# Performance work log

Hardware: AMD Instinct MI355X
Metric: run time of the kernel (lower is better)

## Reference

```python
import jax, jax.numpy as jnp
import numpy as np

EPS = 1e-5

def _causal_conv(x, w):
    # x: [B, Cin, S], w: [Cout, Cin, K]; left-pad by K-1 for causality
    k = w.shape[-1]
    x = jnp.pad(x, ((0, 0), (0, 0), (k - 1, 0)))
    return jax.lax.conv_general_dilated(x, w, (1,), 'VALID',
                                        dimension_numbers=('NCH', 'OIH', 'NCH'))

def _activate_norm(x):
    # relu -> mean-center over last axis -> scaled L2 normalize over last axis
    x = jax.nn.relu(x)
    x = x - x.mean(-1, keepdims=True)
    n = x.shape[-1]
    denom = (jnp.sqrt(jnp.sum(x * x, axis=-1, keepdims=True)) + EPS) * (n ** -0.5)
    return x / denom

def _feed_forward(x, w0, w1, w2):
    x = _causal_conv(x, w0)
    x = _activate_norm(x)
    x = _causal_conv(x, w1)
    x = _activate_norm(x)
    return _causal_conv(x, w2)

def setup_inputs() -> dict:
    key = jax.random.key(0)
    B, F, S = 4, 1024, 2048
    I, K = 2048, 5
    ks = jax.random.split(key, 12)
    def w(k, shape):
        fan_in = shape[1] * shape[2]
        return jax.random.normal(k, shape, jnp.float32) * (fan_in ** -0.5)
    inp = jax.random.normal(ks[0], (B, F, S), jnp.float32)
    pos_embd = jax.random.normal(ks[1], (1, F, S), jnp.float32) * 0.02
    divisor = jax.random.uniform(ks[2], (1, F, S), jnp.float32) + 0.5  # bounded away from 0
    return {
        'inp': inp, 'pos_embd': pos_embd, 'divisor': divisor,
        'dw0': w(ks[3], (I, F, 1)), 'dw1': w(ks[4], (I, I, K)), 'dw2': w(ks[5], (F, I, 1)),
        'sw0': w(ks[6], (I, F, 1)), 'sw1': w(ks[7], (I, I, K)), 'sw2': w(ks[8], (F, I, 1)),
        'hw0': w(ks[9], (I, F, 1)), 'hw1': w(ks[10], (I, I, K)), 'hw2': w(ks[11], (F, I, 1)),
    }

def reference(inp, pos_embd, divisor, dw0, dw1, dw2, sw0, sw1, sw2, hw0, hw1, hw2):
    out = inp + pos_embd
    depth = _feed_forward(out, dw0, dw1, dw2)
    scale = _feed_forward(out, sw0, sw1, sw2)
    shift = _feed_forward(out, hw0, hw1, hw2)
    # linear attention: cumsum over dim 1 (as in source), divide, scale/shift, norm, residual
    return inp + _activate_norm(jnp.cumsum(depth, axis=1) / divisor * scale + shift)
```

## Files before the change

### kernel.cpp

```cpp
#include <hip/hip_runtime.h>
#include <math.h>

#define BSZ 4
#define FCH 1024
#define SEQ 2048
#define ICH 2048
#define KW  5
#define EPSV 1e-5f
#define RPAD 2244
#define NCHUNK 16

typedef __attribute__((ext_vector_type(8))) short bf16x8;
typedef __attribute__((ext_vector_type(4))) float f32x4;
typedef __attribute__((ext_vector_type(4))) unsigned short us4;

__device__ __forceinline__ unsigned short f2bf(float f) {
  union { float f; unsigned u; } v; v.f = f;
  unsigned r = v.u + 0x7fff + ((v.u >> 16) & 1);
  return (unsigned short)(r >> 16);
}

__device__ __forceinline__ void gload_lds16(const void* g, void* l) {
  __builtin_amdgcn_global_load_lds(
      (const __attribute__((address_space(1))) void*)g,
      (__attribute__((address_space(3))) void*)l, 16, 0, 0);
}

__global__ __launch_bounds__(256) void addpos_T_kernel(
    const float* __restrict__ inp, const float* __restrict__ pos,
    unsigned short* __restrict__ X)
{
  __shared__ float t[64][65];
  const int s0 = blockIdx.x * 64, f0 = blockIdx.y * 64, b = blockIdx.z;
  const int a = threadIdx.x & 63, g = threadIdx.x >> 6;
  const float* ib = inp + (size_t)b * FCH * SEQ;
#pragma unroll
  for (int i = 0; i < 16; ++i) {
    const size_t o = (size_t)(f0 + g + i * 4) * SEQ + s0 + a;
    t[a][g + i * 4] = ib[o] + pos[o];
  }
  __syncthreads();
#pragma unroll
  for (int i = 0; i < 16; ++i)
    X[(size_t)b * RPAD * FCH + (size_t)(4 + s0 + g + i * 4) * FCH + f0 + a] =
        f2bf(t[g + i * 4][a]);
}

__global__ __launch_bounds__(256) void zero_xpad_kernel(unsigned short* __restrict__ X)
{
  const int i = blockIdx.x * 256 + threadIdx.x;
  const int b = i / (4 * FCH);
  const int r = i % (4 * FCH);
  X[(size_t)b * RPAD * FCH + r] = 0;
}

__global__ __launch_bounds__(256) void transpose_div_kernel(
    const float* __restrict__ D, float* __restrict__ O)
{
  __shared__ float t[64][65];
  const int s0 = blockIdx.x * 64, f0 = blockIdx.y * 64;
  const int a = threadIdx.x & 63, g = threadIdx.x >> 6;
#pragma unroll
  for (int i = 0; i < 16; ++i)
    t[a][g + i * 4] = D[(size_t)(f0 + g + i * 4) * SEQ + s0 + a];
  __syncthreads();
#pragma unroll
  for (int i = 0; i < 16; ++i)
    O[(size_t)(s0 + g + i * 4) * FCH + f0 + a] = t[g + i * 4][a];
}

__global__ __launch_bounds__(256) void cast_bf_kernel(
    const float* __restrict__ I, unsigned short* __restrict__ O)
{
  const size_t i = ((size_t)blockIdx.x * 256 + threadIdx.x) * 4;
  const float4 v = *(const float4*)(I + i);
  us4 o; o.x = f2bf(v.x); o.y = f2bf(v.y); o.z = f2bf(v.z); o.w = f2bf(v.w);
  *(us4*)(O + i) = o;
}

__global__ __launch_bounds__(256) void cast_w1_kernel(
    const float* __restrict__ W, unsigned short* __restrict__ O)
{
  const int c = blockIdx.x * 256 + threadIdx.x;
  const int m = blockIdx.y;
  const float* s = W + ((size_t)m * ICH + c) * KW;
#pragma unroll
  for (int k = 0; k < KW; ++k)
    O[((size_t)k * ICH + m) * ICH + c] = f2bf(s[k]);
}

template <int BN, int NTAPS>
__global__ __launch_bounds__(512, 2) void gemm256_kernel(
    const unsigned short* __restrict__ A, const unsigned short* __restrict__ W,
    float* __restrict__ C, int M, int K)
{
  extern __shared__ __align__(16) char lds[];
  constexpr int ABYTES = 32768;
  constexpr int BBYTES = BN * 128;
  constexpr int BUF = ABYTES + BBYTES;
  constexpr int WN  = BN / 4;
  constexpr int JF  = BN / 64;
  constexpr int JF2 = BN / 128;

  const int tid = threadIdx.x;
  const int ln  = tid & 63;
  const int wv  = tid >> 6;
  const int wr  = wv >> 2;
  const int wc  = wv & 3;
  const int l15 = ln & 15;
  const int lhi = ln >> 4;

  const int s0 = blockIdx.x * 256;
  const int m0 = blockIdx.y * BN;
  const int b  = blockIdx.z;

  const char* Ab = (const char*)(A + (size_t)b * RPAD * K);
  const char* Wb = (const char*)W;
  const size_t MK = (size_t)M * K;
  const int KT = K >> 6;

  const int scs  = (((tid & 7) ^ ((tid >> 3) & 7)) << 4);
  const int rxor = (l15 & 7) << 4;
  const int cbx0 = (lhi * 16) ^ rxor;
  const int cbx1 = (lhi * 16 + 64) ^ rxor;

  f32x4 acc[8][JF] = {};

  auto STAGE = [&](int t, int k0, int pb) {
    const int roff = (NTAPS == 1) ? 4 : t;
    char* dst = lds + pb * BUF;
#pragma unroll
    for (int q = 0; q < 4; ++q) {
      const int row = (q * 512 + tid) >> 3;
      gload_lds16(Ab + (size_t)(s0 + row + roff) * ((size_t)K * 2) +
                      (size_t)(k0 * 2 + scs),
                  dst + q * 8192 + tid * 16);
    }
#pragma unroll
    for (int q = 0; q < BN / 64; ++q) {
      const int row = (q * 512 + tid) >> 3;
      gload_lds16(Wb + ((size_t)t * MK + (size_t)(m0 + row) * K + k0) * 2 + scs,
                  dst + ABYTES + q * 8192 + tid * 16);
    }
  };

  auto COMPUTE = [&](int pb) {
    const char* bb = lds + pb * BUF;
#pragma unroll
    for (int ih = 0; ih < 2; ++ih) {
      bf16x8 af[4][2];
#pragma unroll
      for (int i = 0; i < 4; ++i) {
        const int r = (wr * 128 + ih * 64 + i * 16 + l15) * 128;
        af[i][0] = *(const bf16x8*)(bb + r + cbx0);
        af[i][1] = *(const bf16x8*)(bb + r + cbx1);
      }
#pragma unroll
      for (int jh = 0; jh < 2; ++jh) {
        bf16x8 bfr[JF2][2];
#pragma unroll
        for (int j = 0; j < JF2; ++j) {
          const int r = ABYTES + (wc * WN + jh * (WN / 2) + j * 16 + l15) * 128;
          bfr[j][0] = *(const bf16x8*)(bb + r + cbx0);
          bfr[j][1] = *(const bf16x8*)(bb + r + cbx1);
        }
        __builtin_amdgcn_s_setprio(1);
#pragma unroll
        for (int i = 0; i < 4; ++i)
#pragma unroll
          for (int j = 0; j < JF2; ++j) {
            acc[ih * 4 + i][jh * JF2 + j] = __builtin_amdgcn_mfma_f32_16x16x32_bf16(
                af[i][0], bfr[j][0], acc[ih * 4 + i][jh * JF2 + j], 0, 0, 0);
            acc[ih * 4 + i][jh * JF2 + j] = __builtin_amdgcn_mfma_f32_16x16x32_bf16(
                af[i][1], bfr[j][1], acc[ih * 4 + i][jh * JF2 + j], 0, 0, 0);
          }
        __builtin_amdgcn_s_setprio(0);
      }
    }
  };

  STAGE(0, 0, 0);
  asm volatile("s_waitcnt vmcnt(0)" ::: "memory");
  __syncthreads();
  int p = 0;
  for (int t = 0; t < NTAPS; ++t) {
    for (int kt = 0; kt < KT; ++kt) {
      int ntp = t, nk = kt + 1;
      if (nk == KT) { nk = 0; ++ntp; }
      if (ntp < NTAPS) STAGE(ntp, nk * 64, p ^ 1);
      COMPUTE(p);
      asm volatile("s_waitcnt vmcnt(0)" ::: "memory");
      __syncthreads();
      p ^= 1;
    }
  }

  float* Cb = C + (size_t)b * SEQ * M;
#pragma unroll
  for (int i = 0; i < 8; ++i) {
    const int sb = s0 + wr * 128 + i * 16 + lhi * 4;
#pragma unroll
    for (int j = 0; j < JF; ++j) {
      const int m = m0 + wc * WN + j * 16 + l15;
#pragma unroll
      for (int r = 0; r < 4; ++r)
        Cb[(size_t)(sb + r) * M + m] = acc[i][j][r];
    }
  }
}

__global__ __launch_bounds__(256) void colred_kernel(
    const float* __restrict__ Cf, float* __restrict__ P1,
    float* __restrict__ P2, int M)
{
  const int b = blockIdx.z;
  const int mi = threadIdx.x & 63;
  const int sg = threadIdx.x >> 6;
  const int m = blockIdx.x * 64 + mi;
  const int s0 = blockIdx.y * 128;
  const float* src = Cf + ((size_t)b * SEQ + s0) * M + m;
  float sum = 0.f, sq = 0.f;
  for (int s = sg; s < 128; s += 4) {
    const float x = fmaxf(src[(size_t)s * M], 0.f);
    sum += x; sq += x * x;
  }
  __shared__ float rs[4][64], rq[4][64];
  rs[sg][mi] = sum; rq[sg][mi] = sq;
  __syncthreads();
  if (sg == 0) {
    const size_t o = ((size_t)b * NCHUNK + blockIdx.y) * M + m;
    P1[o] = rs[0][mi] + rs[1][mi] + rs[2][mi] + rs[3][mi];
    P2[o] = rq[0][mi] + rq[1][mi] + rq[2][mi] + rq[3][mi];
  }
}

__global__ __launch_bounds__(256) void colfin_kernel(
    const float* __restrict__ P1, const float* __restrict__ P2,
    float* __restrict__ MS, int M)
{
  const int i = blockIdx.x * 256 + threadIdx.x;
  const int b = i / M, m = i % M;
  float S1 = 0.f, S2 = 0.f;
#pragma unroll
  for (int c = 0; c < NCHUNK; ++c) {
    S1 += P1[((size_t)b * NCHUNK + c) * M + m];
    S2 += P2[((size_t)b * NCHUNK + c) * M + m];
  }
  const float mean = S1 * (1.f / SEQ);
  const float ss = fmaxf(S2 - SEQ * mean * mean, 0.f);
  const float scl = sqrtf((float)SEQ) / (sqrtf(ss) + EPSV);
  MS[((size_t)b * 2 + 0) * M + m] = mean;
  MS[((size_t)b * 2 + 1) * M + m] = scl;
}

__global__ __launch_bounds__(256) void colapply_kernel(
    const float* __restrict__ Cf, const float* __restrict__ MS,
    unsigned short* __restrict__ Ob, int M)
{
  const int b = blockIdx.z;
  const int mi = threadIdx.x & 63;
  const int sg = threadIdx.x >> 6;
  const int m = blockIdx.x * 64 + mi;
  const int s0 = blockIdx.y * 128;
  const float mean = MS[((size_t)b * 2 + 0) * M + m];
  const float scl  = MS[((size_t)b * 2 + 1) * M + m];
  const float* src = Cf + ((size_t)b * SEQ + s0) * M + m;
  unsigned short* dst = Ob + ((size_t)b * RPAD + 4 + s0) * M + m;
  if (blockIdx.y == 0 && sg == 0) {
#pragma unroll
    for (int r = 0; r < 4; ++r) Ob[((size_t)b * RPAD + r) * M + m] = 0;
  }
  for (int s = sg; s < 128; s += 4)
    dst[(size_t)s * M] = f2bf((fmaxf(src[(size_t)s * M], 0.f) - mean) * scl);
}

__global__ __launch_bounds__(256) void combine_kernel(
    float* __restrict__ Dp, const float* __restrict__ divT,
    const float* __restrict__ Sc, const float* __restrict__ Sh)
{
  const int row = blockIdx.x * 4 + (threadIdx.x >> 6);
  const int b = row >> 11, s = row & 2047;
  const int ln = threadIdx.x & 63;
  const size_t base = ((size_t)b * SEQ + s) * FCH;
  const float* dv = divT + (size_t)s * FCH;
  float carry = 0.f;
  for (int c0 = 0; c0 < FCH; c0 += 64) {
    float x = Dp[base + c0 + ln];
#pragma unroll
    for (int d = 1; d < 64; d <<= 1) {
      const float t = __shfl_up(x, d, 64);
      if (ln >= d) x += t;
    }
    x += carry;
    carry = __shfl(x, 63, 64);
    Dp[base + c0 + ln] = x / dv[c0 + ln] * Sc[base + c0 + ln] + Sh[base + c0 + ln];
  }
}

__global__ __launch_bounds__(256) void final_apply_kernel(
    const float* __restrict__ Df, const float* __restrict__ MS,
    const float* __restrict__ inp, float* __restrict__ out)
{
  __shared__ float tile[64][65];
  const int b = blockIdx.z;
  const int s0 = blockIdx.x * 64, f0 = blockIdx.y * 64;
  const int a = threadIdx.x & 63, g = threadIdx.x >> 6;
  const float mean = MS[((size_t)b * 2 + 0) * FCH + f0 + a];
  const float scl  = MS[((size_t)b * 2 + 1) * FCH + f0 + a];
#pragma unroll
  for (int i = 0; i < 16; ++i) {
    const int s = g + i * 4;
    const float x = fmaxf(Df[((size_t)b * SEQ + s0 + s) * FCH + f0 + a], 0.f);
    tile[s][a] = (x - mean) * scl;
  }
  __syncthreads();
#pragma unroll
  for (int i = 0; i < 16; ++i) {
    const int f = g + i * 4;
    const size_t o = ((size_t)b * FCH + f0 + f) * SEQ + s0 + a;
    out[o] = inp[o] + tile[a][f];
  }
}

extern "C" void kernel_launch(void* const* d_in, const int* in_sizes, int n_in,
                              void* d_out, int out_size, void* d_ws, size_t ws_size,
                              hipStream_t stream)
{
  const float* inp     = (const float*)d_in[0];
  const float* pos     = (const float*)d_in[1];
  const float* divisor = (const float*)d_in[2];
  const float* w_[9];
  for (int i = 0; i < 9; ++i) w_[i] = (const float*)d_in[3 + i];
  float* out = (float*)d_out;

  char* p = (char*)d_ws;
  float*          divT = (float*)p;          p += (size_t)SEQ * FCH * 4;
  unsigned short* Xbf  = (unsigned short*)p; p += (size_t)BSZ * RPAD * FCH * 2;
  unsigned short* T0b  = (unsigned short*)p; p += (size_t)BSZ * RPAD * ICH * 2;
  float*          Cf   = (float*)p;          p += (size_t)BSZ * SEQ * ICH * 4;
  float*          Df   = (float*)p;          p += (size_t)BSZ * SEQ * FCH * 4;
  float*          Sf   = (float*)p;          p += (size_t)BSZ * SEQ * FCH * 4;
  float*          Hf   = (float*)p;          p += (size_t)BSZ * SEQ * FCH * 4;
  unsigned short* w0b  = (unsigned short*)p; p += (size_t)ICH * FCH * 2;
  unsigned short* w1b  = (unsigned short*)p; p += (size_t)KW * ICH * ICH * 2;
  unsigned short* w2b  = (unsigned short*)p; p += (size_t)FCH * ICH * 2;
  float*          P1   = (float*)p;          p += (size_t)BSZ * NCHUNK * ICH * 4;
  float*          P2   = (float*)p;          p += (size_t)BSZ * NCHUNK * ICH * 4;
  float*          MS   = (float*)p;          p += (size_t)BSZ * 2 * ICH * 4;

  hipFuncSetAttribute((const void*)gemm256_kernel<256, 1>,
                      hipFuncAttributeMaxDynamicSharedMemorySize, 131072);
  hipFuncSetAttribute((const void*)gemm256_kernel<256, 5>,
                      hipFuncAttributeMaxDynamicSharedMemorySize, 131072);
  hipFuncSetAttribute((const void*)gemm256_kernel<128, 1>,
                      hipFuncAttributeMaxDynamicSharedMemorySize, 98304);

  zero_xpad_kernel<<<BSZ * 4 * FCH / 256, 256, 0, stream>>>(Xbf);
  addpos_T_kernel<<<dim3(SEQ / 64, FCH / 64, BSZ), 256, 0, stream>>>(inp, pos, Xbf);
  transpose_div_kernel<<<dim3(SEQ / 64, FCH / 64), 256, 0, stream>>>(divisor, divT);

  auto act_norm = [&](const float* src, unsigned short* dst, int M) {
    colred_kernel<<<dim3(M / 64, NCHUNK, BSZ), 256, 0, stream>>>(src, P1, P2, M);
    colfin_kernel<<<(BSZ * M) / 256, 256, 0, stream>>>(P1, P2, MS, M);
    colapply_kernel<<<dim3(M / 64, NCHUNK, BSZ), 256, 0, stream>>>(src, MS, dst, M);
  };

  auto run_ff = [&](const float* w0, const float* w1, const float* w2, float* dst) {
    cast_bf_kernel<<<(ICH * FCH) / 1024, 256, 0, stream>>>(w0, w0b);
    cast_w1_kernel<<<dim3(ICH / 256, ICH), 256, 0, stream>>>(w1, w1b);
    cast_bf_kernel<<<(FCH * ICH) / 1024, 256, 0, stream>>>(w2, w2b);
    gemm256_kernel<256, 1><<<dim3(SEQ / 256, ICH / 256, BSZ), 512, 131072, stream>>>(
        Xbf, w0b, Cf, ICH, FCH);
    act_norm(Cf, T0b, ICH);
    gemm256_kernel<256, 5><<<dim3(SEQ / 256, ICH / 256, BSZ), 512, 131072, stream>>>(
        T0b, w1b, Cf, ICH, ICH);
    act_norm(Cf, T0b, ICH);
    gemm256_kernel<128, 1><<<dim3(SEQ / 256, FCH / 128, BSZ), 512, 98304, stream>>>(
        T0b, w2b, dst, FCH, ICH);
  };

  run_ff(w_[0], w_[1], w_[2], Df);
  run_ff(w_[3], w_[4], w_[5], Sf);
  run_ff(w_[6], w_[7], w_[8], Hf);

  combine_kernel<<<(BSZ * SEQ) / 4, 256, 0, stream>>>(Df, divT, Sf, Hf);

  colred_kernel<<<dim3(FCH / 64, NCHUNK, BSZ), 256, 0, stream>>>(Df, P1, P2, FCH);
  colfin_kernel<<<(BSZ * FCH) / 256, 256, 0, stream>>>(P1, P2, MS, FCH);
  final_apply_kernel<<<dim3(SEQ / 64, FCH / 64, BSZ), 256, 0, stream>>>(
      Df, MS, inp, out);
}
```

Before: 1.339 ms.

## Fuse ReLU and column statistics into GEMM epilogue, store intermediates as bf16

The first two GEMMs of each feed-forward now apply ReLU in their epilogue, write bf16 instead of fp32, and reduce per-column sum and sum-of-squares across the block. Partial sums are combined via shuffles and LDS and written per 256-row chunk. This removes the separate colred pass over the intermediate and halves the intermediate's write and read traffic. The cost is a heavier GEMM epilogue with an extra block barrier, and the statistics are taken from the fp32 values while the apply step reads bf16-rounded values, which adds a little rounding error.

```diff
diff --git a/kernel.cpp b/kernel.cpp
--- a/kernel.cpp
+++ b/kernel.cpp
@@ -8,7 +8,7 @@
 #define KW  5
 #define EPSV 1e-5f
 #define RPAD 2244
-#define NCHUNK 16
+#define NCHF 16
 
 typedef __attribute__((ext_vector_type(8))) short bf16x8;
 typedef __attribute__((ext_vector_type(4))) float f32x4;
@@ -19,6 +19,9 @@
   unsigned r = v.u + 0x7fff + ((v.u >> 16) & 1);
   return (unsigned short)(r >> 16);
 }
+__device__ __forceinline__ float bf2f(unsigned short u) {
+  union { unsigned u; float f; } v; v.u = (unsigned)u << 16; return v.f;
+}
 
 __device__ __forceinline__ void gload_lds16(const void* g, void* l) {
   __builtin_amdgcn_global_load_lds(
@@ -89,10 +92,11 @@
     O[((size_t)k * ICH + m) * ICH + c] = f2bf(s[k]);
 }
 
-template <int BN, int NTAPS>
+template <int BN, int NTAPS, int BF16OUT>
 __global__ __launch_bounds__(512, 2) void gemm256_kernel(
     const unsigned short* __restrict__ A, const unsigned short* __restrict__ W,
-    float* __restrict__ C, int M, int K)
+    void* __restrict__ Cv, int M, int K,
+    float* __restrict__ P1, float* __restrict__ P2)
 {
   extern __shared__ __align__(16) char lds[];
   constexpr int ABYTES = 32768;
@@ -195,16 +199,61 @@
     }
   }
 
-  float* Cb = C + (size_t)b * SEQ * M;
-#pragma unroll
-  for (int i = 0; i < 8; ++i) {
-    const int sb = s0 + wr * 128 + i * 16 + lhi * 4;
+  if constexpr (BF16OUT) {
+    unsigned short* Cb = (unsigned short*)Cv + (size_t)b * SEQ * M;
+    float S[JF] = {}, Q[JF] = {};
+#pragma unroll
+    for (int i = 0; i < 8; ++i) {
+      const int sb = s0 + wr * 128 + i * 16 + lhi * 4;
+#pragma unroll
+      for (int j = 0; j < JF; ++j) {
+        const int m = m0 + wc * WN + j * 16 + l15;
+#pragma unroll
+        for (int r = 0; r < 4; ++r) {
+          const float x = fmaxf(acc[i][j][r], 0.f);
+          S[j] += x; Q[j] += x * x;
+          Cb[(size_t)(sb + r) * M + m] = f2bf(x);
+        }
+      }
+    }
 #pragma unroll
     for (int j = 0; j < JF; ++j) {
-      const int m = m0 + wc * WN + j * 16 + l15;
-#pragma unroll
-      for (int r = 0; r < 4; ++r)
-        Cb[(size_t)(sb + r) * M + m] = acc[i][j][r];
+      S[j] += __shfl_xor(S[j], 16, 64); S[j] += __shfl_xor(S[j], 32, 64);
+      Q[j] += __shfl_xor(Q[j], 16, 64); Q[j] += __shfl_xor(Q[j], 32, 64);
+    }
+    float* SL = (float*)lds;
+    float* QL = SL + 2 * 4 * JF * 16;
+    if (lhi == 0) {
+#pragma unroll
+      for (int j = 0; j < JF; ++j) {
+        SL[((wr * 4 + wc) * JF + j) * 16 + l15] = S[j];
+        QL[((wr * 4 + wc) * JF + j) * 16 + l15] = Q[j];
+      }
+    }
+    __syncthreads();
+    if (wr == 0 && lhi == 0) {
+#pragma unroll
+      for (int j = 0; j < JF; ++j) {
+        const int m = m0 + wc * WN + j * 16 + l15;
+        const size_t o = ((size_t)b * (SEQ / 256) + blockIdx.x) * M + m;
+        P1[o] = SL[((0 * 4 + wc) * JF + j) * 16 + l15] +
+                SL[((1 * 4 + wc) * JF + j) * 16 + l15];
+        P2[o] = QL[((0 * 4 + wc) * JF + j) * 16 + l15] +
+                QL[((1 * 4 + wc) * JF + j) * 16 + l15];
+      }
+    }
+  } else {
+    float* Cb = (float*)Cv + (size_t)b * SEQ * M;
+#pragma unroll
+    for (int i = 0; i < 8; ++i) {
+      const int sb = s0 + wr * 128 + i * 16 + lhi * 4;
+#pragma unroll
+      for (int j = 0; j < JF; ++j) {
+        const int m = m0 + wc * WN + j * 16 + l15;
+#pragma unroll
+        for (int r = 0; r < 4; ++r)
+          Cb[(size_t)(sb + r) * M + m] = acc[i][j][r];
+      }
     }
   }
 }
@@ -228,7 +277,7 @@
   rs[sg][mi] = sum; rq[sg][mi] = sq;
   __syncthreads();
   if (sg == 0) {
-    const size_t o = ((size_t)b * NCHUNK + blockIdx.y) * M + m;
+    const size_t o = ((size_t)b * NCHF + blockIdx.y) * M + m;
     P1[o] = rs[0][mi] + rs[1][mi] + rs[2][mi] + rs[3][mi];
     P2[o] = rq[0][mi] + rq[1][mi] + rq[2][mi] + rq[3][mi];
   }
@@ -236,15 +285,14 @@
 
 __global__ __launch_bounds__(256) void colfin_kernel(
     const float* __restrict__ P1, const float* __restrict__ P2,
-    float* __restrict__ MS, int M)
+    float* __restrict__ MS, int M, int nchunk)
 {
   const int i = blockIdx.x * 256 + threadIdx.x;
   const int b = i / M, m = i % M;
   float S1 = 0.f, S2 = 0.f;
-#pragma unroll
-  for (int c = 0; c < NCHUNK; ++c) {
-    S1 += P1[((size_t)b * NCHUNK + c) * M + m];
-    S2 += P2[((size_t)b * NCHUNK + c) * M + m];
+  for (int c = 0; c < nchunk; ++c) {
+    S1 += P1[((size_t)b * nchunk + c) * M + m];
+    S2 += P2[((size_t)b * nchunk + c) * M + m];
   }
   const float mean = S1 * (1.f / SEQ);
   const float ss = fmaxf(S2 - SEQ * mean * mean, 0.f);
@@ -254,7 +302,7 @@
 }
 
 __global__ __launch_bounds__(256) void colapply_kernel(
-    const float* __restrict__ Cf, const float* __restrict__ MS,
+    const unsigned short* __restrict__ Cf, const float* __restrict__ MS,
     unsigned short* __restrict__ Ob, int M)
 {
   const int b = blockIdx.z;
@@ -264,14 +312,14 @@
   const int s0 = blockIdx.y * 128;
   const float mean = MS[((size_t)b * 2 + 0) * M + m];
   const float scl  = MS[((size_t)b * 2 + 1) * M + m];
-  const float* src = Cf + ((size_t)b * SEQ + s0) * M + m;
+  const unsigned short* src = Cf + ((size_t)b * SEQ + s0) * M + m;
   unsigned short* dst = Ob + ((size_t)b * RPAD + 4 + s0) * M + m;
   if (blockIdx.y == 0 && sg == 0) {
 #pragma unroll
     for (int r = 0; r < 4; ++r) Ob[((size_t)b * RPAD + r) * M + m] = 0;
   }
   for (int s = sg; s < 128; s += 4)
-    dst[(size_t)s * M] = f2bf((fmaxf(src[(size_t)s * M], 0.f) - mean) * scl);
+    dst[(size_t)s * M] = f2bf((bf2f(src[(size_t)s * M]) - mean) * scl);
 }
 
 __global__ __launch_bounds__(256) void combine_kernel(
@@ -337,46 +385,45 @@
   float*          divT = (float*)p;          p += (size_t)SEQ * FCH * 4;
   unsigned short* Xbf  = (unsigned short*)p; p += (size_t)BSZ * RPAD * FCH * 2;
   unsigned short* T0b  = (unsigned short*)p; p += (size_t)BSZ * RPAD * ICH * 2;
-  float*          Cf   = (float*)p;          p += (size_t)BSZ * SEQ * ICH * 4;
+  unsigned short* Cfb  = (unsigned short*)p; p += (size_t)BSZ * SEQ * ICH * 2;
   float*          Df   = (float*)p;          p += (size_t)BSZ * SEQ * FCH * 4;
   float*          Sf   = (float*)p;          p += (size_t)BSZ * SEQ * FCH * 4;
   float*          Hf   = (float*)p;          p += (size_t)BSZ * SEQ * FCH * 4;
   unsigned short* w0b  = (unsigned short*)p; p += (size_t)ICH * FCH * 2;
   unsigned short* w1b  = (unsigned short*)p; p += (size_t)KW * ICH * ICH * 2;
   unsigned short* w2b  = (unsigned short*)p; p += (size_t)FCH * ICH * 2;
-  float*          P1   = (float*)p;          p += (size_t)BSZ * NCHUNK * ICH * 4;
-  float*          P2   = (float*)p;          p += (size_t)BSZ * NCHUNK * ICH * 4;
+  float*          P1   = (float*)p;          p += (size_t)BSZ * NCHF * ICH * 4;
+  float*          P2   = (float*)p;          p += (size_t)BSZ * NCHF * ICH * 4;
   float*          MS   = (float*)p;          p += (size_t)BSZ * 2 * ICH * 4;
 
-  hipFuncSetAttribute((const void*)gemm256_kernel<256, 1>,
+  hipFuncSetAttribute((const void*)gemm256_kernel<256, 1, 1>,
                       hipFuncAttributeMaxDynamicSharedMemorySize, 131072);
-  hipFuncSetAttribute((const void*)gemm256_kernel<256, 5>,
+  hipFuncSetAttribute((const void*)gemm256_kernel<256, 5, 1>,
                       hipFuncAttributeMaxDynamicSharedMemorySize, 131072);
-  hipFuncSetAttribute((const void*)gemm256_kernel<128, 1>,
+  hipFuncSetAttribute((const void*)gemm256_kernel<128, 1, 0>,
                       hipFuncAttributeMaxDynamicSharedMemorySize, 98304);
 
   zero_xpad_kernel<<<BSZ * 4 * FCH / 256, 256, 0, stream>>>(Xbf);
   addpos_T_kernel<<<dim3(SEQ / 64, FCH / 64, BSZ), 256, 0, stream>>>(inp, pos, Xbf);
   transpose_div_kernel<<<dim3(SEQ / 64, FCH / 64), 256, 0, stream>>>(divisor, divT);
 
-  auto act_norm = [&](const float* src, unsigned short* dst, int M) {
-    colred_kernel<<<dim3(M / 64, NCHUNK, BSZ), 256, 0, stream>>>(src, P1, P2, M);
-    colfin_kernel<<<(BSZ * M) / 256, 256, 0, stream>>>(P1, P2, MS, M);
-    colapply_kernel<<<dim3(M / 64, NCHUNK, BSZ), 256, 0, stream>>>(src, MS, dst, M);
+  auto act_norm = [&](unsigned short* dst, int M) {
+    colfin_kernel<<<(BSZ * M) / 256, 256, 0, stream>>>(P1, P2, MS, M, 8);
+    colapply_kernel<<<dim3(M / 64, NCHF, BSZ), 256, 0, stream>>>(Cfb, MS, dst, M);
   };
 
   auto run_ff = [&](const float* w0, const float* w1, const float* w2, float* dst) {
     cast_bf_kernel<<<(ICH * FCH) / 1024, 256, 0, stream>>>(w0, w0b);
     cast_w1_kernel<<<dim3(ICH / 256, ICH), 256, 0, stream>>>(w1, w1b);
     cast_bf_kernel<<<(FCH * ICH) / 1024, 256, 0, stream>>>(w2, w2b);
-    gemm256_kernel<256, 1><<<dim3(SEQ / 256, ICH / 256, BSZ), 512, 131072, stream>>>(
-        Xbf, w0b, Cf, ICH, FCH);
-    act_norm(Cf, T0b, ICH);
-    gemm256_kernel<256, 5><<<dim3(SEQ / 256, ICH / 256, BSZ), 512, 131072, stream>>>(
-        T0b, w1b, Cf, ICH, ICH);
-    act_norm(Cf, T0b, ICH);
-    gemm256_kernel<128, 1><<<dim3(SEQ / 256, FCH / 128, BSZ), 512, 98304, stream>>>(
-        T0b, w2b, dst, FCH, ICH);
+    gemm256_kernel<256, 1, 1><<<dim3(SEQ / 256, ICH / 256, BSZ), 512, 131072, stream>>>(
+        Xbf, w0b, Cfb, ICH, FCH, P1, P2);
+    act_norm(T0b, ICH);
+    gemm256_kernel<256, 5, 1><<<dim3(SEQ / 256, ICH / 256, BSZ), 512, 131072, stream>>>(
+        T0b, w1b, Cfb, ICH, ICH, P1, P2);
+    act_norm(T0b, ICH);
+    gemm256_kernel<128, 1, 0><<<dim3(SEQ / 256, FCH / 128, BSZ), 512, 98304, stream>>>(
+        T0b, w2b, dst, FCH, ICH, P1, P2);
   };
 
   run_ff(w_[0], w_[1], w_[2], Df);
@@ -385,8 +432,8 @@
 
   combine_kernel<<<(BSZ * SEQ) / 4, 256, 0, stream>>>(Df, divT, Sf, Hf);
 
-  colred_kernel<<<dim3(FCH / 64, NCHUNK, BSZ), 256, 0, stream>>>(Df, P1, P2, FCH);
-  colfin_kernel<<<(BSZ * FCH) / 256, 256, 0, stream>>>(P1, P2, MS, FCH);
+  colred_kernel<<<dim3(FCH / 64, NCHF, BSZ), 256, 0, stream>>>(Df, P1, P2, FCH);
+  colfin_kernel<<<(BSZ * FCH) / 256, 256, 0, stream>>>(P1, P2, MS, FCH, NCHF);
   final_apply_kernel<<<dim3(SEQ / 64, FCH / 64, BSZ), 256, 0, stream>>>(
       Df, MS, inp, out);
 }
```

New measurement: 1.239 ms. -7.5%, faster.
